# Performance work log

Hardware: AMD Instinct MI355X
Metric: run time of the kernel (lower is better)

## Reference

```python
import jax, jax.numpy as jnp
import numpy as np

OVERLAP = 0.5
N_BOXES = 8192
FEATURE_LEN = 10


def _nms_keep(bboxes, scores, overlap):
    """Vectorized-equivalent of the sequential NMS while-loop.

    bboxes: [N,4] in (x, y, w, h) format (matches xmax = x + w in source).
    Returns a boolean keep mask over the original N boxes. Greedy order is
    descending score (source sorts ascending and pops the last element).
    Boxes with IoU > overlap w.r.t. a kept box are suppressed (iou.le(overlap)
    survives in the source).
    """
    N = bboxes.shape[0]
    x1 = bboxes[:, 0]
    y1 = bboxes[:, 1]
    x2 = bboxes[:, 0] + bboxes[:, 2]
    y2 = bboxes[:, 1] + bboxes[:, 3]
    area = (x2 - x1) * (y2 - y1)

    order = jnp.argsort(scores)[::-1]  # descending score
    xs1, ys1 = x1[order], y1[order]
    xs2, ys2 = x2[order], y2[order]
    ar = area[order]

    # Pairwise intersection in sorted order (same clamp math as the source).
    ix1 = jnp.maximum(xs1[:, None], xs1[None, :])
    iy1 = jnp.maximum(ys1[:, None], ys1[None, :])
    ix2 = jnp.minimum(xs2[:, None], xs2[None, :])
    iy2 = jnp.minimum(ys2[:, None], ys2[None, :])
    inter = jnp.clip(ix2 - ix1, 0.0) * jnp.clip(iy2 - iy1, 0.0)
    iou = inter / (ar[:, None] + ar[None, :] - inter)

    later = jnp.arange(N)[None, :] > jnp.arange(N)[:, None]
    sup = (iou > overlap) & later  # row i suppresses later j

    def body(i, state):
        keep, removed = state
        alive = jnp.logical_not(removed[i])
        keep = keep.at[i].set(alive)
        removed = removed | (alive & sup[i])
        return keep, removed

    keep_sorted, _ = jax.lax.fori_loop(
        0, N, body, (jnp.zeros(N, bool), jnp.zeros(N, bool)))
    # map back to original box indices
    return jnp.zeros(N, bool).at[order].set(keep_sorted)


def _bbox_regression(features, W, b, rect):
    """bounding_box_regression: t = sigmoid(Linear(features)); shift boxes."""
    t = jax.nn.sigmoid(features @ W + b)  # [N,4]
    x = jnp.clip(t[:, 0] * rect[:, 2] + rect[:, 0], 0.0)
    y = jnp.clip(t[:, 1] * rect[:, 3] + rect[:, 1], 0.0)
    w = rect[:, 2] * jnp.exp(t[:, 2])
    h = rect[:, 3] * jnp.exp(t[:, 3])
    return jnp.stack([x, y, w, h], axis=-1)


def setup_inputs() -> dict:
    key = jax.random.key(0)
    k0, k1, k2, k3, k4 = jax.random.split(key, 5)
    N = N_BOXES
    bboxes = jax.random.uniform(k0, (N, 4), jnp.float32)  # (x,y,w,h) in [0,1)
    scores = jax.random.uniform(k1, (N,), jnp.float32)
    features = jax.random.normal(k2, (N, FEATURE_LEN), jnp.float32)
    W = jax.random.normal(k3, (FEATURE_LEN, 4), jnp.float32) * 0.1
    b = jax.random.normal(k4, (4,), jnp.float32) * 0.1
    return {"bboxes": bboxes, "scores": scores, "features": features,
            "W": W, "b": b, "width": 1024, "height": 1024}


def reference(bboxes, scores, features, W, b, width, height):
    keep = _nms_keep(bboxes, scores, OVERLAP)
    reg = _bbox_regression(features, W, b, bboxes)
    # transform_bounding_box with start_points=(0,0), scales=(1,1):
    # scales normalized coords back to pixel space.
    scale = jnp.array([width, height, width, height], jnp.float32)
    out = reg * scale * keep[:, None].astype(reg.dtype)
    return out
```

## Files before the change

### kernel.cpp

```cpp
#include <hip/hip_runtime.h>
#include <hip/hip_bf16.h>

#define N_BOXES 8192
#define NW 128
#define FEAT 10
#define NSLOT 4

typedef unsigned long long u64;
typedef unsigned int u32;

__device__ __forceinline__ void barrier_nodrain() {
    asm volatile("s_waitcnt lgkmcnt(0)" ::: "memory");
    __builtin_amdgcn_sched_barrier(0);
    __builtin_amdgcn_s_barrier();
    __builtin_amdgcn_sched_barrier(0);
    asm volatile("" ::: "memory");
}

__global__ void rank_scatter_kernel(const float* __restrict__ bboxes,
                                    const float* __restrict__ scores,
                                    float* __restrict__ x1s, float* __restrict__ y1s,
                                    float* __restrict__ x2s, float* __restrict__ y2s,
                                    u32* __restrict__ rank_of) {
    __shared__ float sc[N_BOXES];
    int tid = threadIdx.x;
    for (int t = 0; t < N_BOXES / 256; ++t)
        sc[tid + 256 * t] = scores[tid + 256 * t];
    __syncthreads();
    int k = tid >> 3;
    int s = tid & 7;
    int i = blockIdx.x * 32 + k;
    float si = sc[i];
    int cnt = 0;
    const float4* sc4 = (const float4*)sc;
    int q0 = s * (N_BOXES / 32);
    #pragma unroll 4
    for (int q = q0; q < q0 + N_BOXES / 32; ++q) {
        float4 v = sc4[q];
        int j = 4 * q;
        cnt += (int)((v.x > si) || (v.x == si && j     > i));
        cnt += (int)((v.y > si) || (v.y == si && j + 1 > i));
        cnt += (int)((v.z > si) || (v.z == si && j + 2 > i));
        cnt += (int)((v.w > si) || (v.w == si && j + 3 > i));
    }
    cnt += __shfl_down(cnt, 4, 8);
    cnt += __shfl_down(cnt, 2, 8);
    cnt += __shfl_down(cnt, 1, 8);
    if (s == 0) {
        int r = cnt;
        float x = bboxes[4 * i + 0], y = bboxes[4 * i + 1];
        float w = bboxes[4 * i + 2], h = bboxes[4 * i + 3];
        float x2 = x + w, y2 = y + h;
        x1s[r] = x; y1s[r] = y; x2s[r] = x2; y2s[r] = y2;
        rank_of[i] = (u32)r;
    }
}

__global__ void __launch_bounds__(256) mask_kernel(
        const float* __restrict__ x1s, const float* __restrict__ y1s,
        const float* __restrict__ x2s, const float* __restrict__ y2s,
        u64* __restrict__ RM, u64* __restrict__ TRb) {
    int wv = threadIdx.x >> 6, lane = threadIdx.x & 63;
    int ci = blockIdx.x;
    int cj = blockIdx.y * 4 + wv;
    if (cj < ci) return;
    __shared__ float S[4][4][64];
    int d = cj - ci;
    int ig0 = ci * 64, jg0 = cj * 64;
    if (d <= 3) {
        S[wv][0][lane] = x1s[ig0 + lane];
        S[wv][1][lane] = y1s[ig0 + lane];
        S[wv][2][lane] = x2s[ig0 + lane];
        S[wv][3][lane] = y2s[ig0 + lane];
        int jg = jg0 + lane;
        float jx1 = x1s[jg], jy1 = y1s[jg], jx2 = x2s[jg], jy2 = y2s[jg];
        float jar = (jx2 - jx1) * (jy2 - jy1);
        u64 my = 0, cw = 0;
        for (int ip = 0; ip < 64; ++ip) {
            float ax1 = S[wv][0][ip], ay1 = S[wv][1][ip];
            float ax2 = S[wv][2][ip], ay2 = S[wv][3][ip];
            float aar = (ax2 - ax1) * (ay2 - ay1);
            float xx1 = fmaxf(ax1, jx1);
            float yy1 = fmaxf(ay1, jy1);
            float xx2 = fminf(ax2, jx2);
            float yy2 = fminf(ay2, jy2);
            float iw = fmaxf(xx2 - xx1, 0.0f);
            float ih = fmaxf(yy2 - yy1, 0.0f);
            float inter = iw * ih;
            float uni = aar + jar - inter;
            float iou = __fdiv_rn(inter, uni);
            bool sup = (iou > 0.5f) && (jg > ig0 + ip);
            u64 w = __ballot(sup);
            if (lane == ip) my = w;
            cw |= sup ? (1ull << ip) : 0ull;
        }
        RM[(size_t)(ig0 + lane) * NW + cj] = my;
        TRb[(size_t)d * N_BOXES + jg] = cw;
    } else {
        S[wv][0][lane] = x1s[jg0 + lane];
        S[wv][1][lane] = y1s[jg0 + lane];
        S[wv][2][lane] = x2s[jg0 + lane];
        S[wv][3][lane] = y2s[jg0 + lane];
        int ig = ig0 + lane;
        float ix1 = x1s[ig], iy1 = y1s[ig], ix2 = x2s[ig], iy2 = y2s[ig];
        float iar = (ix2 - ix1) * (iy2 - iy1);
        u64 my = 0;
        for (int jp = 0; jp < 64; ++jp) {
            float jx1 = S[wv][0][jp], jy1 = S[wv][1][jp];
            float jx2 = S[wv][2][jp], jy2 = S[wv][3][jp];
            float jar = (jx2 - jx1) * (jy2 - jy1);
            float xx1 = fmaxf(ix1, jx1);
            float yy1 = fmaxf(iy1, jy1);
            float xx2 = fminf(ix2, jx2);
            float yy2 = fminf(iy2, jy2);
            float iw = fmaxf(xx2 - xx1, 0.0f);
            float ih = fmaxf(yy2 - yy1, 0.0f);
            float inter = iw * ih;
            float uni = iar + jar - inter;
            float iou = __fdiv_rn(inter, uni);
            bool sup = (iou > 0.5f);
            my |= sup ? (1ull << jp) : 0ull;
        }
        RM[(size_t)ig * NW + cj] = my;
    }
}

__global__ void __launch_bounds__(512) nms_reduce_fused(
        const u64* __restrict__ RM, const u64* __restrict__ TRb,
        u64* __restrict__ keepw_g) {
    __shared__ __align__(8) u32 rem32[NW * 2];
    __shared__ u64 keptw[NW];
    __shared__ unsigned char klist[4][64];

    const int tid = threadIdx.x;
    const int wv = tid >> 6, lane = tid & 63;
    const int grp = wv - 1;

    if (tid < NW * 2) rem32[tid] = 0;

    u64 TR0[2], TR1[2], TR2[2], TR3[2];
    u64 kp1 = 0, kp2 = 0, kp3 = 0;
    if (wv == 0) {
        TR0[0] = TRb[lane];
        TR1[0] = TRb[N_BOXES + lane];
        TR2[0] = TRb[2 * N_BOXES + lane];
        TR3[0] = TRb[3 * N_BOXES + lane];
        TR0[1] = TRb[64 + lane];
        TR1[1] = TRb[N_BOXES + 64 + lane];
        TR2[1] = TRb[2 * N_BOXES + 64 + lane];
        TR3[1] = TRb[3 * N_BOXES + 64 + lane];
    }
    u64 H0[2][NSLOT], H1[2][NSLOT];
    u32 Kn[2] = {0, 0};
    __syncthreads();

#define REGION(RC, PAR)                                                         \
  do {                                                                          \
    const int c_ = (RC);                                                        \
    if (wv == 0) {                                                              \
      u64 TD = TR0[PAR], T1f = TR1[PAR], T2f = TR2[PAR], T3f = TR3[PAR];        \
      u64 base = *(const u64*)&rem32[2 * c_];                                   \
      u64 R = base |                                                            \
              __ballot(((T1f & kp1) | (T2f & kp2) | (T3f & kp3)) != 0ull);      \
      u64 K = 0, U = ~R;                                                        \
      bool meU = (U >> lane) & 1;                                               \
      while (U) {                                                               \
        u64 UK = U | K;                                                         \
        u64 nK = __ballot(meU && ((TD & UK) == 0ull));                          \
        K |= nK;                                                                \
        u64 nR = __ballot(meU && ((TD & K) != 0ull));                           \
        U &= ~(K | nR);                                                         \
        meU = (U >> lane) & 1;                                                  \
      }                                                                         \
      bool isk = (K >> lane) & 1;                                               \
      int rnk = __popcll(K & ((1ull << lane) - 1ull));                          \
      if (isk) klist[c_ & 3][rnk] = (unsigned char)lane;                        \
      if (lane == 0) keptw[c_] = K;                                             \
      kp3 = kp2; kp2 = kp1; kp1 = K;                                            \
      if (c_ + 2 < NW) {                                                        \
        TR0[PAR] = TRb[(c_ + 2) * 64 + lane];                                   \
        TR1[PAR] = TRb[N_BOXES + (c_ + 2) * 64 + lane];                         \
        TR2[PAR] = TRb[2 * N_BOXES + (c_ + 2) * 64 + lane];                     \
        TR3[PAR] = TRb[3 * N_BOXES + (c_ + 2) * 64 + lane];                     \
      }                                                                         \
    } else {                                                                    \
               \
      if (c_ >= 3 && Kn[PAR] > 0) {                                             \
        const int wd0 = c_ + 1 + lane;                                          \
        const int wd1 = wd0 + 64;                                               \
        u64 v0 = 0, v1 = 0;                                                     \
        _Pragma("unroll")                                                       \
        for (int s = 0; s < NSLOT; ++s) { v0 |= H0[PAR][s]; v1 |= H1[PAR][s]; } \
        u32 kn = Kn[PAR];                                                       \
        if (kn > 7u * NSLOT) {                               \
          const u32 cpb = (u32)(c_ - 3) * 64u;                                  \
          const unsigned char* kl = klist[(c_ + 1) & 3];                        \
          for (u32 r = 7u * NSLOT + (u32)grp; r < kn; r += 7u) {                \
            const u64* rp = RM + (size_t)(cpb + kl[r]) * NW;                    \
            if (wd0 < NW) v0 |= rp[wd0];                                        \
            if (wd1 < NW) v1 |= rp[wd1];                                        \
          }                                                                     \
        }                                                                       \
        if (wd0 < NW && v0) atomicOr((u64*)&rem32[2 * wd0], v0);                \
        if (wd1 < NW && v1) atomicOr((u64*)&rem32[2 * wd1], v1);                \
      }                                                                         \
                \
      {                                                                         \
        const int cp = c_ - 1;                                                  \
        if (cp >= 0 && c_ + 3 < NW) {                                           \
          u64 KW = keptw[cp];                                                   \
          u32 kn = (u32)__popcll(KW);                                           \
          Kn[PAR] = kn;                                                         \
          const int wi0 = c_ + 3 + lane;                                        \
          const int wi1 = wi0 + 64;                                             \
          const unsigned char* kl = klist[cp & 3];                              \
          const u32 cpb = (u32)cp * 64u;                                        \
          _Pragma("unroll")                                                     \
          for (int s = 0; s < NSLOT; ++s) {                                     \
            H0[PAR][s] = 0; H1[PAR][s] = 0;                                     \
            u32 r = (u32)(s * 7 + grp);                       \
            if (r < kn) {                                                       \
              const u64* rp = RM + (size_t)(cpb + kl[r]) * NW;                  \
              if (wi0 < NW) H0[PAR][s] = rp[wi0];                               \
              if (wi1 < NW) H1[PAR][s] = rp[wi1];                               \
            }                                                                   \
          }                                                                     \
        } else Kn[PAR] = 0;                                                     \
      }                                                                         \
    }                                                                           \
    barrier_nodrain();                                                          \
  } while (0)

    for (int cc = 0; cc < NW; cc += 2) {
        REGION(cc, 0);
        REGION(cc + 1, 1);
    }
#undef REGION

    __syncthreads();
    if (tid < NW) keepw_g[tid] = keptw[tid];
}

__global__ void output_kernel(const float* __restrict__ bboxes,
                              const float* __restrict__ features,
                              const float* __restrict__ Wm, const float* __restrict__ bv,
                              const int* __restrict__ widthp, const int* __restrict__ heightp,
                              const u32* __restrict__ rank_of, const u64* __restrict__ keepw,
                              float* __restrict__ out) {
    int i = blockIdx.x * blockDim.x + threadIdx.x;
    if (i >= N_BOXES) return;
    u32 r = rank_of[i];
    float keep = (float)((keepw[r >> 6] >> (r & 63)) & 1ull);
    float z0 = bv[0], z1 = bv[1], z2 = bv[2], z3 = bv[3];
    #pragma unroll
    for (int m = 0; m < FEAT; ++m) {
        float f = features[i * FEAT + m];
        z0 += f * Wm[m * 4 + 0];
        z1 += f * Wm[m * 4 + 1];
        z2 += f * Wm[m * 4 + 2];
        z3 += f * Wm[m * 4 + 3];
    }
    float t0 = 1.0f / (1.0f + expf(-z0));
    float t1 = 1.0f / (1.0f + expf(-z1));
    float t2 = 1.0f / (1.0f + expf(-z2));
    float t3 = 1.0f / (1.0f + expf(-z3));
    float4 bx = ((const float4*)bboxes)[i];
    float ox = fmaxf(t0 * bx.z + bx.x, 0.0f);
    float oy = fmaxf(t1 * bx.w + bx.y, 0.0f);
    float ow = bx.z * expf(t2);
    float oh = bx.w * expf(t3);
    float sw = (float)(*widthp), sh = (float)(*heightp);
    float4 o;
    o.x = ox * sw * keep;
    o.y = oy * sh * keep;
    o.z = ow * sw * keep;
    o.w = oh * sh * keep;
    ((float4*)out)[i] = o;
}

extern "C" void kernel_launch(void* const* d_in, const int* in_sizes, int n_in,
                              void* d_out, int out_size, void* d_ws, size_t ws_size,
                              hipStream_t stream) {
    const float* bboxes   = (const float*)d_in[0];
    const float* scores   = (const float*)d_in[1];
    const float* features = (const float*)d_in[2];
    const float* Wm       = (const float*)d_in[3];
    const float* bv       = (const float*)d_in[4];
    const int*   widthp   = (const int*)d_in[5];
    const int*   heightp  = (const int*)d_in[6];
    float* out = (float*)d_out;

    char* ws = (char*)d_ws;
    u64* RM      = (u64*)ws;
    u64* TRb     = (u64*)(ws + (size_t)N_BOXES * NW * sizeof(u64));
    float* x1s   = (float*)((char*)TRb + (size_t)4 * N_BOXES * sizeof(u64));
    float* y1s   = x1s + N_BOXES;
    float* x2s   = y1s + N_BOXES;
    float* y2s   = x2s + N_BOXES;
    u32* rank_of = (u32*)(y2s + N_BOXES);
    u64* keepw   = (u64*)(rank_of + N_BOXES);

    rank_scatter_kernel<<<N_BOXES / 32, 256, 0, stream>>>(bboxes, scores,
                                                          x1s, y1s, x2s, y2s, rank_of);
    mask_kernel<<<dim3(NW, NW / 4), 256, 0, stream>>>(x1s, y1s, x2s, y2s, RM, TRb);
    nms_reduce_fused<<<1, 512, 0, stream>>>(RM, TRb, keepw);
    output_kernel<<<N_BOXES / 256, 256, 0, stream>>>(bboxes, features, Wm, bv,
                                                     widthp, heightp, rank_of, keepw, out);
}
```

Baseline: 151.4 us.

## Process two 64-box chunks per barrier region in the serial NMS reduce

The single-block NMS reduction now handles two column chunks per barrier-separated region instead of one, which halves the number of block barriers on the serial critical path. To support this, the mask kernel emits transposed near-diagonal suppression words for up to 5 chunk offsets instead of 3, and the leader wave resolves the odd chunk against the even chunk just computed. Helper waves propagate suppression from two kept lists per region. The cost is more registers, more TRb workspace and more work per region on the leader wave.

Measured after the change: 131.3 us. -13.3%, faster.

```diff
diff --git a/kernel.cpp b/kernel.cpp
--- a/kernel.cpp
+++ b/kernel.cpp
@@ -3,6 +3,7 @@
 
 #define N_BOXES 8192
 #define NW 128
+#define NREG 64
 #define FEAT 10
 #define NSLOT 4
 
@@ -67,7 +68,7 @@
     __shared__ float S[4][4][64];
     int d = cj - ci;
     int ig0 = ci * 64, jg0 = cj * 64;
-    if (d <= 3) {
+    if (d <= 5) {
         S[wv][0][lane] = x1s[ig0 + lane];
         S[wv][1][lane] = y1s[ig0 + lane];
         S[wv][2][lane] = x2s[ig0 + lane];
@@ -125,12 +126,12 @@
     }
 }
 
-__global__ void __launch_bounds__(512) nms_reduce_fused(
+__global__ void __launch_bounds__(512) nms_reduce(
         const u64* __restrict__ RM, const u64* __restrict__ TRb,
         u64* __restrict__ keepw_g) {
     __shared__ __align__(8) u32 rem32[NW * 2];
     __shared__ u64 keptw[NW];
-    __shared__ unsigned char klist[4][64];
+    __shared__ unsigned char klA[4][64], klB[4][64];
 
     const int tid = threadIdx.x;
     const int wv = tid >> 6, lane = tid & 63;
@@ -138,64 +139,107 @@
 
     if (tid < NW * 2) rem32[tid] = 0;
 
-    u64 TR0[2], TR1[2], TR2[2], TR3[2];
-    u64 kp1 = 0, kp2 = 0, kp3 = 0;
+    u64 TDe[2], T1e[2], T2e[2], T3e[2], T4e[2];
+    u64 TDo[2], T1o[2], T2o[2], T3o[2], T4o[2], T5o[2];
+    u64 kp1 = 0, kp2 = 0, kp3 = 0, kp4 = 0;
     if (wv == 0) {
-        TR0[0] = TRb[lane];
-        TR1[0] = TRb[N_BOXES + lane];
-        TR2[0] = TRb[2 * N_BOXES + lane];
-        TR3[0] = TRb[3 * N_BOXES + lane];
-        TR0[1] = TRb[64 + lane];
-        TR1[1] = TRb[N_BOXES + 64 + lane];
-        TR2[1] = TRb[2 * N_BOXES + 64 + lane];
-        TR3[1] = TRb[3 * N_BOXES + 64 + lane];
-    }
-    u64 H0[2][NSLOT], H1[2][NSLOT];
-    u32 Kn[2] = {0, 0};
+        TDe[0] = TRb[lane];
+        T1e[0] = TRb[N_BOXES + lane];
+        T2e[0] = TRb[2 * N_BOXES + lane];
+        T3e[0] = TRb[3 * N_BOXES + lane];
+        T4e[0] = TRb[4 * N_BOXES + lane];
+        TDo[0] = TRb[64 + lane];
+        T1o[0] = TRb[N_BOXES + 64 + lane];
+        T2o[0] = TRb[2 * N_BOXES + 64 + lane];
+        T3o[0] = TRb[3 * N_BOXES + 64 + lane];
+        T4o[0] = TRb[4 * N_BOXES + 64 + lane];
+        T5o[0] = TRb[5 * N_BOXES + 64 + lane];
+    }
+    u64 HA0[NSLOT], HA1[NSLOT], HB0[NSLOT], HB1[NSLOT];
+    u32 KnA = 0, KnB = 0;
     __syncthreads();
 
-#define REGION(RC, PAR)                                                         \
-  do {                                                                          \
-    const int c_ = (RC);                                                        \
-    if (wv == 0) {                                                              \
-      u64 TD = TR0[PAR], T1f = TR1[PAR], T2f = TR2[PAR], T3f = TR3[PAR];        \
-      u64 base = *(const u64*)&rem32[2 * c_];                                   \
-      u64 R = base |                                                            \
-              __ballot(((T1f & kp1) | (T2f & kp2) | (T3f & kp3)) != 0ull);      \
-      u64 K = 0, U = ~R;                                                        \
+#define FIXPOINT(TD, RIN, KOUT)                                                 \
+    {                                                                           \
+      u64 K = 0, U = ~(RIN);                                                    \
       bool meU = (U >> lane) & 1;                                               \
       while (U) {                                                               \
         u64 UK = U | K;                                                         \
-        u64 nK = __ballot(meU && ((TD & UK) == 0ull));                          \
+        u64 nK = __ballot(meU && (((TD) & UK) == 0ull));                        \
         K |= nK;                                                                \
-        u64 nR = __ballot(meU && ((TD & K) != 0ull));                           \
+        u64 nR = __ballot(meU && (((TD) & K) != 0ull));                         \
         U &= ~(K | nR);                                                         \
         meU = (U >> lane) & 1;                                                  \
       }                                                                         \
-      bool isk = (K >> lane) & 1;                                               \
-      int rnk = __popcll(K & ((1ull << lane) - 1ull));                          \
-      if (isk) klist[c_ & 3][rnk] = (unsigned char)lane;                        \
-      if (lane == 0) keptw[c_] = K;                                             \
-      kp3 = kp2; kp2 = kp1; kp1 = K;                                            \
-      if (c_ + 2 < NW) {                                                        \
-        TR0[PAR] = TRb[(c_ + 2) * 64 + lane];                                   \
-        TR1[PAR] = TRb[N_BOXES + (c_ + 2) * 64 + lane];                         \
-        TR2[PAR] = TRb[2 * N_BOXES + (c_ + 2) * 64 + lane];                     \
-        TR3[PAR] = TRb[3 * N_BOXES + (c_ + 2) * 64 + lane];                     \
-      }                                                                         \
+      (KOUT) = K;                                                               \
+    }
+
+#define REGION(Q, PAR)                                                          \
+  do {                                                                          \
+    const int q_ = (Q);                                                         \
+    const int c0 = 2 * q_, c1 = 2 * q_ + 1;                                     \
+    if (wv == 0) {                                                              \
+      if (q_ + 1 < NREG) {                   \
+        const int n0 = (c0 + 2) * 64 + lane, n1 = n0 + 64;                      \
+        TDe[PAR ^ 1] = TRb[n0];                                                 \
+        T1e[PAR ^ 1] = TRb[N_BOXES + n0];                                       \
+        T2e[PAR ^ 1] = TRb[2 * N_BOXES + n0];                                   \
+        T3e[PAR ^ 1] = TRb[3 * N_BOXES + n0];                                   \
+        T4e[PAR ^ 1] = TRb[4 * N_BOXES + n0];                                   \
+        TDo[PAR ^ 1] = TRb[n1];                                                 \
+        T1o[PAR ^ 1] = TRb[N_BOXES + n1];                                       \
+        T2o[PAR ^ 1] = TRb[2 * N_BOXES + n1];                                   \
+        T3o[PAR ^ 1] = TRb[3 * N_BOXES + n1];                                   \
+        T4o[PAR ^ 1] = TRb[4 * N_BOXES + n1];                                   \
+        T5o[PAR ^ 1] = TRb[5 * N_BOXES + n1];                                   \
+      }                                                                         \
+      u64 K0, K1;                                                               \
+      {                                                                         \
+        u64 base0 = *(const u64*)&rem32[2 * c0];                                \
+        u64 R0 = base0 | __ballot(((T1e[PAR] & kp1) | (T2e[PAR] & kp2) |        \
+                                   (T3e[PAR] & kp3) | (T4e[PAR] & kp4)) != 0ull);\
+        FIXPOINT(TDe[PAR], R0, K0);                                             \
+        bool isk = (K0 >> lane) & 1;                                            \
+        int rnk = __popcll(K0 & ((1ull << lane) - 1ull));                       \
+        if (isk) klA[q_ & 3][rnk] = (unsigned char)lane;                        \
+        if (lane == 0) keptw[c0] = K0;                                          \
+      }                                                                         \
+      {                                                                         \
+        u64 base1 = *(const u64*)&rem32[2 * c1];                                \
+        u64 R1 = base1 | __ballot(((T1o[PAR] & K0)  | (T2o[PAR] & kp1) |        \
+                                   (T3o[PAR] & kp2) | (T4o[PAR] & kp3) |        \
+                                   (T5o[PAR] & kp4)) != 0ull);                  \
+        FIXPOINT(TDo[PAR], R1, K1);                                             \
+        bool isk = (K1 >> lane) & 1;                                            \
+        int rnk = __popcll(K1 & ((1ull << lane) - 1ull));                       \
+        if (isk) klB[q_ & 3][rnk] = (unsigned char)lane;                        \
+        if (lane == 0) keptw[c1] = K1;                                          \
+      }                                                                         \
+      kp4 = kp2; kp3 = kp1; kp2 = K0; kp1 = K1;                                 \
     } else {                                                                    \
-               \
-      if (c_ >= 3 && Kn[PAR] > 0) {                                             \
-        const int wd0 = c_ + 1 + lane;                                          \
+                      \
+      if (q_ >= 2 && (KnA | KnB)) {                                             \
+        const int wd0 = 2 * q_ + 1 + lane;                                      \
         const int wd1 = wd0 + 64;                                               \
         u64 v0 = 0, v1 = 0;                                                     \
         _Pragma("unroll")                                                       \
-        for (int s = 0; s < NSLOT; ++s) { v0 |= H0[PAR][s]; v1 |= H1[PAR][s]; } \
-        u32 kn = Kn[PAR];                                                       \
-        if (kn > 7u * NSLOT) {                               \
-          const u32 cpb = (u32)(c_ - 3) * 64u;                                  \
-          const unsigned char* kl = klist[(c_ + 1) & 3];                        \
-          for (u32 r = 7u * NSLOT + (u32)grp; r < kn; r += 7u) {                \
+        for (int s = 0; s < NSLOT; ++s) {                                       \
+          v0 |= HA0[s] | HB0[s];                                                \
+          v1 |= HA1[s] | HB1[s];                                                \
+        }                                                                       \
+        if (KnA > 7u * NSLOT) {                              \
+          const u32 cpb = (u32)(2 * q_ - 4) * 64u;                              \
+          const unsigned char* kl = klA[(q_ - 2) & 3];                          \
+          for (u32 r = 7u * NSLOT + (u32)grp; r < KnA; r += 7u) {               \
+            const u64* rp = RM + (size_t)(cpb + kl[r]) * NW;                    \
+            if (wd0 < NW) v0 |= rp[wd0];                                        \
+            if (wd1 < NW) v1 |= rp[wd1];                                        \
+          }                                                                     \
+        }                                                                       \
+        if (KnB > 7u * NSLOT) {                                                 \
+          const u32 cpb = (u32)(2 * q_ - 3) * 64u;                              \
+          const unsigned char* kl = klB[(q_ - 2) & 3];                          \
+          for (u32 r = 7u * NSLOT + (u32)grp; r < KnB; r += 7u) {               \
             const u64* rp = RM + (size_t)(cpb + kl[r]) * NW;                    \
             if (wd0 < NW) v0 |= rp[wd0];                                        \
             if (wd1 < NW) v1 |= rp[wd1];                                        \
@@ -204,38 +248,44 @@
         if (wd0 < NW && v0) atomicOr((u64*)&rem32[2 * wd0], v0);                \
         if (wd1 < NW && v1) atomicOr((u64*)&rem32[2 * wd1], v1);                \
       }                                                                         \
-                \
+                    \
       {                                                                         \
-        const int cp = c_ - 1;                                                  \
-        if (cp >= 0 && c_ + 3 < NW) {                                           \
-          u64 KW = keptw[cp];                                                   \
-          u32 kn = (u32)__popcll(KW);                                           \
-          Kn[PAR] = kn;                                                         \
-          const int wi0 = c_ + 3 + lane;                                        \
+        const int ib = 2 * q_ + 3;                                              \
+        if (q_ >= 1 && ib < NW) {                                               \
+          const u32 cA = (u32)(2 * q_ - 2) * 64u, cB = cA + 64u;                \
+          KnA = (u32)__popcll(keptw[2 * q_ - 2]);                               \
+          KnB = (u32)__popcll(keptw[2 * q_ - 1]);                               \
+          const int wi0 = ib + lane;                                            \
           const int wi1 = wi0 + 64;                                             \
-          const unsigned char* kl = klist[cp & 3];                              \
-          const u32 cpb = (u32)cp * 64u;                                        \
+          const unsigned char* kla = klA[(q_ - 1) & 3];                         \
+          const unsigned char* klb = klB[(q_ - 1) & 3];                         \
           _Pragma("unroll")                                                     \
           for (int s = 0; s < NSLOT; ++s) {                                     \
-            H0[PAR][s] = 0; H1[PAR][s] = 0;                                     \
+            HA0[s] = 0; HA1[s] = 0; HB0[s] = 0; HB1[s] = 0;                     \
             u32 r = (u32)(s * 7 + grp);                       \
-            if (r < kn) {                                                       \
-              const u64* rp = RM + (size_t)(cpb + kl[r]) * NW;                  \
-              if (wi0 < NW) H0[PAR][s] = rp[wi0];                               \
-              if (wi1 < NW) H1[PAR][s] = rp[wi1];                               \
+            if (r < KnA) {                                                      \
+              const u64* rp = RM + (size_t)(cA + kla[r]) * NW;                  \
+              if (wi0 < NW) HA0[s] = rp[wi0];                                   \
+              if (wi1 < NW) HA1[s] = rp[wi1];                                   \
+            }                                                                   \
+            if (r < KnB) {                                                      \
+              const u64* rp = RM + (size_t)(cB + klb[r]) * NW;                  \
+              if (wi0 < NW) HB0[s] = rp[wi0];                                   \
+              if (wi1 < NW) HB1[s] = rp[wi1];                                   \
             }                                                                   \
           }                                                                     \
-        } else Kn[PAR] = 0;                                                     \
+        } else { KnA = 0; KnB = 0; }                                            \
       }                                                                         \
     }                                                                           \
     barrier_nodrain();                                                          \
   } while (0)
 
-    for (int cc = 0; cc < NW; cc += 2) {
-        REGION(cc, 0);
-        REGION(cc + 1, 1);
+    for (int qq = 0; qq < NREG; qq += 2) {
+        REGION(qq, 0);
+        REGION(qq + 1, 1);
     }
 #undef REGION
+#undef FIXPOINT
 
     __syncthreads();
     if (tid < NW) keepw_g[tid] = keptw[tid];
@@ -293,7 +343,7 @@
     char* ws = (char*)d_ws;
     u64* RM      = (u64*)ws;
     u64* TRb     = (u64*)(ws + (size_t)N_BOXES * NW * sizeof(u64));
-    float* x1s   = (float*)((char*)TRb + (size_t)4 * N_BOXES * sizeof(u64));
+    float* x1s   = (float*)((char*)TRb + (size_t)6 * N_BOXES * sizeof(u64));
     float* y1s   = x1s + N_BOXES;
     float* x2s   = y1s + N_BOXES;
     float* y2s   = x2s + N_BOXES;
@@ -303,7 +353,7 @@
     rank_scatter_kernel<<<N_BOXES / 32, 256, 0, stream>>>(bboxes, scores,
                                                           x1s, y1s, x2s, y2s, rank_of);
     mask_kernel<<<dim3(NW, NW / 4), 256, 0, stream>>>(x1s, y1s, x2s, y2s, RM, TRb);
-    nms_reduce_fused<<<1, 512, 0, stream>>>(RM, TRb, keepw);
+    nms_reduce<<<1, 512, 0, stream>>>(RM, TRb, keepw);
     output_kernel<<<N_BOXES / 256, 256, 0, stream>>>(bboxes, features, Wm, bv,
                                                      widthp, heightp, rank_of, keepw, out);
 }
```

## Replace 8-wave barrier-synchronised NMS reduce with a single-wave register pipeline

Applied to the files above, without the earlier changes.

Rewrites the serial NMS reduction as one 64-lane wavefront. Each lane holds two 64-bit removal words in registers, and rows of kept boxes are prefetched several chunks ahead into register slots, with a zero row used as a dummy. This removes the per-chunk block barriers, the LDS atomics and the cross-wave handoff. The mask kernel now writes a fifth diagonal band of transposed masks so the lookahead can reach back four chunks. The price is that one wave issues all the row loads serially, and register pressure rises with 24 ulonglong2 slots.

Result: slower. 223.4 us (+47.5%).

```diff
diff --git a/kernel.cpp b/kernel.cpp
--- a/kernel.cpp
+++ b/kernel.cpp
@@ -4,18 +4,10 @@
 #define N_BOXES 8192
 #define NW 128
 #define FEAT 10
-#define NSLOT 4
+#define NS 6
 
 typedef unsigned long long u64;
 typedef unsigned int u32;
-
-__device__ __forceinline__ void barrier_nodrain() {
-    asm volatile("s_waitcnt lgkmcnt(0)" ::: "memory");
-    __builtin_amdgcn_sched_barrier(0);
-    __builtin_amdgcn_s_barrier();
-    __builtin_amdgcn_sched_barrier(0);
-    asm volatile("" ::: "memory");
-}
 
 __global__ void rank_scatter_kernel(const float* __restrict__ bboxes,
                                     const float* __restrict__ scores,
@@ -67,7 +59,7 @@
     __shared__ float S[4][4][64];
     int d = cj - ci;
     int ig0 = ci * 64, jg0 = cj * 64;
-    if (d <= 3) {
+    if (d <= 4) {
         S[wv][0][lane] = x1s[ig0 + lane];
         S[wv][1][lane] = y1s[ig0 + lane];
         S[wv][2][lane] = x2s[ig0 + lane];
@@ -125,120 +117,94 @@
     }
 }
 
-__global__ void __launch_bounds__(512) nms_reduce_fused(
+__global__ void __launch_bounds__(64) nms_reduce(
         const u64* __restrict__ RM, const u64* __restrict__ TRb,
-        u64* __restrict__ keepw_g) {
-    __shared__ __align__(8) u32 rem32[NW * 2];
-    __shared__ u64 keptw[NW];
-    __shared__ unsigned char klist[4][64];
-
-    const int tid = threadIdx.x;
-    const int wv = tid >> 6, lane = tid & 63;
-    const int grp = wv - 1;
-
-    if (tid < NW * 2) rem32[tid] = 0;
-
-    u64 TR0[2], TR1[2], TR2[2], TR3[2];
-    u64 kp1 = 0, kp2 = 0, kp3 = 0;
-    if (wv == 0) {
-        TR0[0] = TRb[lane];
-        TR1[0] = TRb[N_BOXES + lane];
-        TR2[0] = TRb[2 * N_BOXES + lane];
-        TR3[0] = TRb[3 * N_BOXES + lane];
-        TR0[1] = TRb[64 + lane];
-        TR1[1] = TRb[N_BOXES + 64 + lane];
-        TR2[1] = TRb[2 * N_BOXES + 64 + lane];
-        TR3[1] = TRb[3 * N_BOXES + 64 + lane];
-    }
-    u64 H0[2][NSLOT], H1[2][NSLOT];
-    u32 Kn[2] = {0, 0};
-    __syncthreads();
-
-#define REGION(RC, PAR)                                                         \
-  do {                                                                          \
-    const int c_ = (RC);                                                        \
-    if (wv == 0) {                                                              \
-      u64 TD = TR0[PAR], T1f = TR1[PAR], T2f = TR2[PAR], T3f = TR3[PAR];        \
-      u64 base = *(const u64*)&rem32[2 * c_];                                   \
-      u64 R = base |                                                            \
-              __ballot(((T1f & kp1) | (T2f & kp2) | (T3f & kp3)) != 0ull);      \
-      u64 K = 0, U = ~R;                                                        \
-      bool meU = (U >> lane) & 1;                                               \
-      while (U) {                                                               \
-        u64 UK = U | K;                                                         \
-        u64 nK = __ballot(meU && ((TD & UK) == 0ull));                          \
-        K |= nK;                                                                \
-        u64 nR = __ballot(meU && ((TD & K) != 0ull));                           \
-        U &= ~(K | nR);                                                         \
-        meU = (U >> lane) & 1;                                                  \
-      }                                                                         \
-      bool isk = (K >> lane) & 1;                                               \
-      int rnk = __popcll(K & ((1ull << lane) - 1ull));                          \
-      if (isk) klist[c_ & 3][rnk] = (unsigned char)lane;                        \
-      if (lane == 0) keptw[c_] = K;                                             \
-      kp3 = kp2; kp2 = kp1; kp1 = K;                                            \
-      if (c_ + 2 < NW) {                                                        \
-        TR0[PAR] = TRb[(c_ + 2) * 64 + lane];                                   \
-        TR1[PAR] = TRb[N_BOXES + (c_ + 2) * 64 + lane];                         \
-        TR2[PAR] = TRb[2 * N_BOXES + (c_ + 2) * 64 + lane];                     \
-        TR3[PAR] = TRb[3 * N_BOXES + (c_ + 2) * 64 + lane];                     \
-      }                                                                         \
-    } else {                                                                    \
-               \
-      if (c_ >= 3 && Kn[PAR] > 0) {                                             \
-        const int wd0 = c_ + 1 + lane;                                          \
-        const int wd1 = wd0 + 64;                                               \
-        u64 v0 = 0, v1 = 0;                                                     \
-        _Pragma("unroll")                                                       \
-        for (int s = 0; s < NSLOT; ++s) { v0 |= H0[PAR][s]; v1 |= H1[PAR][s]; } \
-        u32 kn = Kn[PAR];                                                       \
-        if (kn > 7u * NSLOT) {                               \
-          const u32 cpb = (u32)(c_ - 3) * 64u;                                  \
-          const unsigned char* kl = klist[(c_ + 1) & 3];                        \
-          for (u32 r = 7u * NSLOT + (u32)grp; r < kn; r += 7u) {                \
-            const u64* rp = RM + (size_t)(cpb + kl[r]) * NW;                    \
-            if (wd0 < NW) v0 |= rp[wd0];                                        \
-            if (wd1 < NW) v1 |= rp[wd1];                                        \
-          }                                                                     \
-        }                                                                       \
-        if (wd0 < NW && v0) atomicOr((u64*)&rem32[2 * wd0], v0);                \
-        if (wd1 < NW && v1) atomicOr((u64*)&rem32[2 * wd1], v1);                \
-      }                                                                         \
-                \
-      {                                                                         \
-        const int cp = c_ - 1;                                                  \
-        if (cp >= 0 && c_ + 3 < NW) {                                           \
-          u64 KW = keptw[cp];                                                   \
-          u32 kn = (u32)__popcll(KW);                                           \
-          Kn[PAR] = kn;                                                         \
-          const int wi0 = c_ + 3 + lane;                                        \
-          const int wi1 = wi0 + 64;                                             \
-          const unsigned char* kl = klist[cp & 3];                              \
-          const u32 cpb = (u32)cp * 64u;                                        \
-          _Pragma("unroll")                                                     \
-          for (int s = 0; s < NSLOT; ++s) {                                     \
-            H0[PAR][s] = 0; H1[PAR][s] = 0;                                     \
-            u32 r = (u32)(s * 7 + grp);                       \
-            if (r < kn) {                                                       \
-              const u64* rp = RM + (size_t)(cpb + kl[r]) * NW;                  \
-              if (wi0 < NW) H0[PAR][s] = rp[wi0];                               \
-              if (wi1 < NW) H1[PAR][s] = rp[wi1];                               \
-            }                                                                   \
-          }                                                                     \
-        } else Kn[PAR] = 0;                                                     \
-      }                                                                         \
-    }                                                                           \
-    barrier_nodrain();                                                          \
+        const u64* __restrict__ zrow, u64* __restrict__ keepw_g) {
+    const int lane = threadIdx.x;
+    u64 rem0 = 0, rem1 = 0;
+    u64 kp1 = 0, kp2 = 0, kp3 = 0, kp4 = 0;
+    ulonglong2 HA[NS], HB[NS], HC[NS], HD[NS];
+    #pragma unroll
+    for (int s = 0; s < NS; ++s) {
+        HA[s].x = 0; HA[s].y = 0; HB[s].x = 0; HB[s].y = 0;
+        HC[s].x = 0; HC[s].y = 0; HD[s].x = 0; HD[s].y = 0;
+    }
+    u64 TDa, T1a, T2a, T3a, T4a, TDb, T1b, T2b, T3b, T4b;
+    u64 TDc, T1c, T2c, T3c, T4c, TDd, T1d, T2d, T3d, T4d;
+
+#define LOADTR(CC, TD_, T1_, T2_, T3_, T4_)                                    \
+    { int a_ = (CC) * 64 + lane;                                               \
+      TD_ = TRb[a_];                T1_ = TRb[N_BOXES + a_];                   \
+      T2_ = TRb[2 * N_BOXES + a_];  T3_ = TRb[3 * N_BOXES + a_];               \
+      T4_ = TRb[4 * N_BOXES + a_]; }
+
+    LOADTR(0, TDa, T1a, T2a, T3a, T4a);
+    LOADTR(1, TDb, T1b, T2b, T3b, T4b);
+    LOADTR(2, TDc, T1c, T2c, T3c, T4c);
+    LOADTR(3, TDd, T1d, T2d, T3d, T4d);
+
+    const ulonglong2* zr = (const ulonglong2*)zrow + lane;
+
+#define CHUNK(C, HS, TD_, T1_, T2_, T3_, T4_)                                  \
+  do {                                                                         \
+    const int c_ = (C);                                                        \
+              \
+    _Pragma("unroll")                                                          \
+    for (int s = 0; s < NS; ++s) { rem0 |= HS[s].x; rem1 |= HS[s].y; }         \
+                       \
+    u64 rsel = (c_ & 1) ? rem1 : rem0;                                         \
+    u32 blo = __shfl((u32)rsel, c_ >> 1);                                      \
+    u32 bhi = __shfl((u32)(rsel >> 32), c_ >> 1);                              \
+    u64 base = ((u64)bhi << 32) | (u64)blo;                                    \
+    u64 ext = (T1_ & kp1) | (T2_ & kp2) | (T3_ & kp3) | (T4_ & kp4);           \
+    u64 R = base | __ballot(ext != 0ull);                                      \
+    u64 K = 0, U = ~R;                                                         \
+    bool meU = (U >> lane) & 1;                                                \
+    while (U) {                                                                \
+      u64 UK = U | K;                                                          \
+      u64 nK = __ballot(meU && ((TD_ & UK) == 0ull));                          \
+      K |= nK;                                                                 \
+      u64 nR = __ballot(meU && ((TD_ & K) != 0ull));                           \
+      U &= ~(K | nR);                                                          \
+      meU = (U >> lane) & 1;                                                   \
+    }                                                                          \
+    if (lane == 0) keepw_g[c_] = K;                                            \
+    kp4 = kp3; kp3 = kp2; kp2 = kp1; kp1 = K;                                  \
+                 \
+    { int cn_ = (c_ + 4 < NW) ? c_ + 4 : NW - 1;                               \
+      LOADTR(cn_, TD_, T1_, T2_, T3_, T4_); }                                  \
+              \
+    u64 kk = (c_ < NW - 5) ? K : 0ull;                                         \
+    _Pragma("unroll")                                                          \
+    for (int s = 0; s < NS; ++s) {                                             \
+      const ulonglong2* rp = zr;                                               \
+      if (kk) { int b = __builtin_ctzll(kk); kk &= kk - 1;                     \
+                rp = (const ulonglong2*)(RM + (size_t)(c_ * 64 + b) * NW)      \
+                     + lane; }                                                 \
+      HS[s] = *rp;                                                             \
+    }                                                                          \
+    while (kk) {            \
+      ulonglong2 T_[8];                                                        \
+      _Pragma("unroll")                                                        \
+      for (int s = 0; s < 8; ++s) {                                            \
+        T_[s].x = 0; T_[s].y = 0;                                              \
+        if (kk) { int b = __builtin_ctzll(kk); kk &= kk - 1;                   \
+                  T_[s] = *((const ulonglong2*)(RM +                           \
+                            (size_t)(c_ * 64 + b) * NW) + lane); }             \
+      }                                                                        \
+      _Pragma("unroll")                                                        \
+      for (int s = 0; s < 8; ++s) { rem0 |= T_[s].x; rem1 |= T_[s].y; }        \
+    }                                                                          \
   } while (0)
 
-    for (int cc = 0; cc < NW; cc += 2) {
-        REGION(cc, 0);
-        REGION(cc + 1, 1);
-    }
-#undef REGION
-
-    __syncthreads();
-    if (tid < NW) keepw_g[tid] = keptw[tid];
+    for (int cc = 0; cc < NW; cc += 4) {
+        CHUNK(cc,     HA, TDa, T1a, T2a, T3a, T4a);
+        CHUNK(cc + 1, HB, TDb, T1b, T2b, T3b, T4b);
+        CHUNK(cc + 2, HC, TDc, T1c, T2c, T3c, T4c);
+        CHUNK(cc + 3, HD, TDd, T1d, T2d, T3d, T4d);
+    }
+#undef CHUNK
+#undef LOADTR
 }
 
 __global__ void output_kernel(const float* __restrict__ bboxes,
@@ -293,17 +259,20 @@
     char* ws = (char*)d_ws;
     u64* RM      = (u64*)ws;
     u64* TRb     = (u64*)(ws + (size_t)N_BOXES * NW * sizeof(u64));
-    float* x1s   = (float*)((char*)TRb + (size_t)4 * N_BOXES * sizeof(u64));
+    u64* zrow    = (u64*)((char*)TRb + (size_t)5 * N_BOXES * sizeof(u64));
+    float* x1s   = (float*)((char*)zrow + NW * sizeof(u64));
     float* y1s   = x1s + N_BOXES;
     float* x2s   = y1s + N_BOXES;
     float* y2s   = x2s + N_BOXES;
     u32* rank_of = (u32*)(y2s + N_BOXES);
     u64* keepw   = (u64*)(rank_of + N_BOXES);
 
+    hipMemsetAsync(zrow, 0, NW * sizeof(u64), stream);
+
     rank_scatter_kernel<<<N_BOXES / 32, 256, 0, stream>>>(bboxes, scores,
                                                           x1s, y1s, x2s, y2s, rank_of);
     mask_kernel<<<dim3(NW, NW / 4), 256, 0, stream>>>(x1s, y1s, x2s, y2s, RM, TRb);
-    nms_reduce_fused<<<1, 512, 0, stream>>>(RM, TRb, keepw);
+    nms_reduce<<<1, 64, 0, stream>>>(RM, TRb, zrow, keepw);
     output_kernel<<<N_BOXES / 256, 256, 0, stream>>>(bboxes, features, Wm, bv,
                                                      widthp, heightp, rank_of, keepw, out);
 }
```
